# Kernel tuning notes

Hardware: AMD Instinct MI355X
Metric: run time of the kernel (lower is better)

The kernel has to match this reference:

```python
import jax, jax.numpy as jnp
import numpy as np

B, C, RED, H, RANK = 32768, 1024, 4, 4, 16
CH = C // RED          # 256 hidden width after gated down-projection
DH = CH // H           # 64 head dim
RATIO = 0.5            # residual_ratio
LN_EPS = 1e-5


def setup_inputs() -> dict:
    key = jax.random.key(0)
    ks = iter(jax.random.split(key, 32))
    n = lambda shape, s=0.02: jax.random.normal(next(ks), shape, jnp.float32) * s
    return {
        "x": jax.random.normal(next(ks), (B, C), jnp.float32),
        # LayerNorm(c_in)
        "ln_g": jnp.ones((C,), jnp.float32),
        "ln_b": jnp.zeros((C,), jnp.float32),
        # gated linear: down_proj / gate_proj  (stored [in, out])
        "Wd": n((C, CH)), "bd": jnp.zeros((CH,), jnp.float32),
        "Wg": n((C, CH)), "bg": jnp.zeros((CH,), jnp.float32),
        # depthwise Conv1d(CH, CH, k=1, groups=CH) on length-1 seq -> per-channel affine
        "dw_w": n((CH,), 1.0), "dw_b": jnp.zeros((CH,), jnp.float32),
        # LightFNN: Linear-GELU-Linear
        "W1": n((CH, CH)), "b1": jnp.zeros((CH,), jnp.float32),
        "W2": n((CH, CH)), "b2": jnp.zeros((CH,), jnp.float32),
        # MHSA (seq_len = 1)
        "Wq": n((CH, CH)), "bq": jnp.zeros((CH,), jnp.float32),
        "Wk": n((CH, CH)), "bk": jnp.zeros((CH,), jnp.float32),
        "Wv": n((CH, CH)), "bv": jnp.zeros((CH,), jnp.float32),
        "Wo": n((CH, CH)), "bo": jnp.zeros((CH,), jnp.float32),
        # up_proj
        "Wu": n((CH, C)), "bu": jnp.zeros((C,), jnp.float32),
        # LoRA (bias-free)
        "Wld": n((C, RANK)), "Wlu": n((RANK, C)),
    }


def reference(x, ln_g, ln_b, Wd, bd, Wg, bg, dw_w, dw_b,
              W1, b1, W2, b2, Wq, bq, Wk, bk, Wv, bv, Wo, bo,
              Wu, bu, Wld, Wlu):
    residual = x
    # LayerNorm
    mu = jnp.mean(x, axis=-1, keepdims=True)
    var = jnp.mean(jnp.square(x - mu), axis=-1, keepdims=True)
    h = (x - mu) * jax.lax.rsqrt(var + LN_EPS) * ln_g + ln_b
    # gated linear unit
    h = (h @ Wd + bd) * jax.nn.sigmoid(h @ Wg + bg)          # [B, CH]
    # depthwise conv over length-1 sequence == per-channel affine
    h = h * dw_w + dw_b
    # light FFN
    h = jax.nn.gelu(h @ W1 + b1) @ W2 + b2
    # seq_len-1 self-attention: softmax over a single key is 1 => out = Wo(v)
    q = (h @ Wq + bq).reshape(B, H, DH)
    k = (h @ Wk + bk).reshape(B, H, DH)
    v = (h @ Wv + bv).reshape(B, H, DH)
    scores = jnp.sum(q * k, axis=-1, keepdims=True) / jnp.sqrt(jnp.float32(DH))  # [B,H,1]
    attn = jax.nn.softmax(scores, axis=-1)                   # == ones
    h = (attn * v).reshape(B, CH) @ Wo + bo
    # up projection + LoRA
    h = h @ Wu + bu                                          # [B, C]
    h = h + (h @ Wld) @ Wlu
    # dropout is identity at inference; weighted residual mix
    return RATIO * h + (1.0 - RATIO) * residual
```

## Files before the change

kernel.cpp:

```cpp
#include <hip/hip_runtime.h>
#include <hip/hip_bf16.h>
#include <stdint.h>


typedef float f32x4 __attribute__((ext_vector_type(4)));
typedef __bf16 bf16x8 __attribute__((ext_vector_type(8)));
typedef unsigned short u16x8 __attribute__((ext_vector_type(8)));
typedef unsigned short u16x4 __attribute__((ext_vector_type(4)));

#define LN_EPS 1e-5f

__device__ __forceinline__ unsigned short f2bf(float f) {
  unsigned int u = __float_as_uint(f);
  u += 0x7fffu + ((u >> 16) & 1u);
  return (unsigned short)(u >> 16);
}

__device__ __forceinline__ void bar_lds() {
  asm volatile("s_waitcnt lgkmcnt(0)\n\ts_barrier" ::: "memory");
}

__global__ __launch_bounds__(256) void k_prep1(
    const float* __restrict__ ln_g, const float* __restrict__ ln_b,
    const float* __restrict__ Wd, const float* __restrict__ Wg,
    const float* __restrict__ dw_w, const float* __restrict__ dw_b,
    const float* __restrict__ W1, const float* __restrict__ b1,
    const float* __restrict__ W2, const float* __restrict__ b2,
    const float* __restrict__ Wv, const float* __restrict__ Wo,
    const float* __restrict__ Wu,
    unsigned short* __restrict__ PGd, unsigned short* __restrict__ PGg,
    unsigned short* __restrict__ PW1, unsigned short* __restrict__ PWv,
    unsigned short* __restrict__ PWo, unsigned short* __restrict__ PWu,
    float* __restrict__ gdvA, float* __restrict__ ggvA,
    float* __restrict__ bdA, float* __restrict__ bgA,
    float* __restrict__ b1p, float* __restrict__ A0) {
  __shared__ float S[32][257];
  const int b = blockIdx.x, tid = threadIdx.x;

  if (b < 120) {
    const float* src; const float* scale = nullptr; unsigned short* dst;
    int N = 256, kc, NT = 16, nt0 = 0;
    bool csum = false; float* accg_ = nullptr; float* accb_ = nullptr;
    if (b < 32)      { src = Wd; scale = ln_g; dst = PGd; kc = b;      csum = true; accg_ = gdvA; accb_ = bdA; }
    else if (b < 64) { src = Wg; scale = ln_g; dst = PGg; kc = b - 32; csum = true; accg_ = ggvA; accb_ = bgA; }
    else if (b < 72) { src = W1; scale = dw_w; dst = PW1; kc = b - 64; }
    else if (b < 80) { src = Wv; dst = PWv; kc = b - 72; }
    else if (b < 88) { src = Wo; dst = PWo; kc = b - 80; }
    else { int idx = b - 88; kc = idx >> 2; nt0 = (idx & 3) * 16; src = Wu; dst = PWu; N = 1024; NT = 64; }
    const int n0 = nt0 * 16;
    float csg = 0.f, csb = 0.f;
    for (int r = 0; r < 32; ++r) {
      int k = kc * 32 + r;
      float raw = src[(size_t)k * N + n0 + tid];
      float v = scale ? scale[k] * raw : raw;
      S[r][tid] = v;
      if (csum) { csg += v; csb += ln_b[k] * raw; }
    }
    if (csum) { atomicAdd(&accg_[tid], csg); atomicAdd(&accb_[tid], csb); }
    __syncthreads();
    const int ntL = tid >> 4;
    #pragma unroll
    for (int c = 0; c < 4; ++c) {
      int lane = (tid * 4 + c) & 63;
      int kb = (lane >> 4) * 8, nl = ntL * 16 + (lane & 15);
      u16x8 o;
      #pragma unroll
      for (int j = 0; j < 8; ++j) o[j] = f2bf(S[kb + j][nl]);
      *(u16x8*)(dst + ((size_t)(kc * NT + nt0 + ntL) * 64 + lane) * 8) = o;
    }
  } else if (b == 120) {
    float s = 0.f;
    for (int k = 0; k < 256; ++k) s += dw_b[k] * W1[k * 256 + tid];
    b1p[tid] = b1[tid] + s;
  } else {
    int rb = b - 121;
    for (int it = 0; it < 16; ++it) {
      int el = rb * 4096 + it * 256 + tid;
      int row = el >> 8, col = el & 255;
      float v = (row < 256) ? W2[el] : ((row == 256) ? b2[col] : 0.f);
      A0[el] = v;
    }
  }
}

__global__ __launch_bounds__(256) void k_gemm272(
    const float* __restrict__ A, const unsigned short* __restrict__ PB,
    float* __restrict__ C, const float* __restrict__ bias, int NT) {
  __shared__ unsigned short XA[512];
  const int tid = threadIdx.x;
  const int w = tid >> 6, l = tid & 63, q = l >> 4, m15 = l & 15;
  const int r0 = blockIdx.x * 16, ncg = blockIdx.y, N = NT * 16;

  const int srow = tid >> 4, kk = (tid & 15) * 2;
  const int xaidx = ((kk >> 3) * 16 + srow) * 8 + (kk & 7);
  const float* arow = A + (size_t)(r0 + srow) * 256 + kk;

  f32x4 acc[4];
  const f32x4 zero4 = {0.f, 0.f, 0.f, 0.f};
  #pragma unroll
  for (int i = 0; i < 4; ++i) acc[i] = zero4;

  for (int kc = 0; kc < 8; ++kc) {
    float2 v = *(const float2*)(arow + kc * 32);
    u16x4 hv; hv[0] = f2bf(v.x); hv[1] = f2bf(v.y); hv[2] = 0; hv[3] = 0;
    XA[xaidx] = hv[0]; XA[xaidx + 1] = hv[1];
    __syncthreads();
    bf16x8 af = *(const bf16x8*)&XA[l * 8];
    #pragma unroll
    for (int i = 0; i < 4; ++i) {
      bf16x8 bf = *(const bf16x8*)(PB + ((size_t)(kc * NT + ncg * 16 + w * 4 + i) * 64 + l) * 8);
      acc[i] = __builtin_amdgcn_mfma_f32_16x16x32_bf16(af, bf, acc[i], 0, 0, 0);
    }
    __syncthreads();
  }
  #pragma unroll
  for (int i = 0; i < 4; ++i) {
    int col = ncg * 256 + (w * 4 + i) * 16 + m15;
    #pragma unroll
    for (int r = 0; r < 4; ++r) {
      int grow = r0 + q * 4 + r;
      float v = acc[i][r];
      if (grow == 256) v += bias[col];
      C[(size_t)grow * N + col] = v;
    }
  }
}

__global__ __launch_bounds__(256) void k_lora_m4(
    const float* __restrict__ M3, const float* __restrict__ Wld,
    float* __restrict__ M4) {
  __shared__ float RED[256 * 16];
  __shared__ float RED2[16 * 16];
  const int r = blockIdx.x, tid = threadIdx.x;
  const float* mrow = M3 + (size_t)r * 1024;
  float p[16];
  #pragma unroll
  for (int c = 0; c < 16; ++c) p[c] = 0.f;
  #pragma unroll
  for (int k = 0; k < 4; ++k) {
    int n = tid + k * 256;
    float m = mrow[n];
    const float* wl = Wld + n * 16;
    #pragma unroll
    for (int c = 0; c < 16; ++c) p[c] += m * wl[c];
  }
  #pragma unroll
  for (int c = 0; c < 16; ++c) RED[tid * 16 + c] = p[c];
  __syncthreads();
  {
    const int c = tid & 15, g = tid >> 4;
    float s = 0.f;
    #pragma unroll
    for (int i = 0; i < 16; ++i) s += RED[(g * 16 + i) * 16 + c];
    RED2[g * 16 + c] = s;
  }
  __syncthreads();
  if (tid < 16) {
    float s = 0.f;
    #pragma unroll
    for (int g = 0; g < 16; ++g) s += RED2[g * 16 + tid];
    M4[r * 16 + tid] = s;
  }
}

__global__ __launch_bounds__(256) void k_packwc2(
    const float* __restrict__ M3, const float* __restrict__ M4,
    const float* __restrict__ Wlu, unsigned short* __restrict__ PWc,
    float* __restrict__ bcomb) {
  const int b = blockIdx.x, tid = threadIdx.x;
  if (b < 64) {
    __shared__ float M4L[32 * 16];
    __shared__ float WL[16 * 128];
    __shared__ unsigned short TL[32 * 132];
    const int kc = b >> 3, ccol = (b & 7) * 128;
    M4L[tid] = M4[(size_t)kc * 512 + tid];
    M4L[tid + 256] = M4[(size_t)kc * 512 + 256 + tid];
    #pragma unroll
    for (int i = 0; i < 8; ++i) {
      int el = tid + i * 256;
      int s = el >> 7, n = el & 127;
      WL[el] = Wlu[(size_t)s * 1024 + ccol + n];
    }
    __syncthreads();
    const int r = tid >> 3, c0 = (tid & 7) * 16;
    const float* mrow = M3 + (size_t)(kc * 32 + r) * 1024 + ccol + c0;
    float acc[16];
    #pragma unroll
    for (int c = 0; c < 16; ++c) acc[c] = mrow[c];
    #pragma unroll
    for (int s = 0; s < 16; ++s) {
      float m = M4L[r * 16 + s];
      #pragma unroll
      for (int c = 0; c < 16; ++c) acc[c] += m * WL[s * 128 + c0 + c];
    }
    #pragma unroll
    for (int c = 0; c < 16; ++c) TL[r * 132 + c0 + c] = f2bf(acc[c]);
    __syncthreads();
    const int ntL = tid >> 5;
    #pragma unroll
    for (int hlf = 0; hlf < 2; ++hlf) {
      int lane = (tid & 31) + hlf * 32;
      int kb = (lane >> 4) * 8, nl = ntL * 16 + (lane & 15);
      u16x8 o;
      #pragma unroll
      for (int j = 0; j < 8; ++j) o[j] = TL[(kb + j) * 132 + nl];
      *(u16x8*)(PWc + ((size_t)(kc * 64 + (b & 7) * 8 + ntL) * 64 + lane) * 8) = o;
    }
  } else {
    __shared__ float s16[16];
    if (tid < 16) s16[tid] = M4[256 * 16 + tid];
    __syncthreads();
    const float* bc3 = M3 + (size_t)256 * 1024;
    #pragma unroll
    for (int c = 0; c < 4; ++c) {
      int n = tid + c * 256;
      float v = bc3[n];
      #pragma unroll
      for (int s = 0; s < 16; ++s) v += s16[s] * Wlu[s * 1024 + n];
      bcomb[n] = v;
    }
  }
}

__global__ __launch_bounds__(512, 4) void k_main(
    const float* __restrict__ x,
    const unsigned short* __restrict__ PGd, const unsigned short* __restrict__ PGg,
    const unsigned short* __restrict__ PW1, const unsigned short* __restrict__ PWc,
    const float* __restrict__ gdvA, const float* __restrict__ ggvA,
    const float* __restrict__ bdA, const float* __restrict__ bgA,
    const float* __restrict__ bd, const float* __restrict__ bg,
    const float* __restrict__ b1p, const float* __restrict__ bcomb,
    float* __restrict__ out) {
  __shared__ unsigned short XA[2][2048];
  __shared__ unsigned short HBUF[16384];
  __shared__ float SMS[1024];
  __shared__ float MURS[128];
  __shared__ float OBUF[16 * 260];

  const int tid = threadIdx.x;
  const int w = tid >> 6, l = tid & 63, q = l >> 4, m15 = l & 15;
  const int row0 = blockIdx.x * 64;

  float gdc[2], ggc[2], bdc[2], bgc[2], b1c[2];
  #pragma unroll
  for (int i = 0; i < 2; ++i) {
    int col = w * 32 + i * 16 + m15;
    gdc[i] = gdvA[col]; ggc[i] = ggvA[col];
    bdc[i] = bdA[col] + bd[col];
    bgc[i] = bgA[col] + bg[col];
    b1c[i] = b1p[col];
  }

  f32x4 accd[4][2], accg[4][2];
  const f32x4 zero4 = {0.f, 0.f, 0.f, 0.f};
  #pragma unroll
  for (int mt = 0; mt < 4; ++mt)
    #pragma unroll
    for (int i = 0; i < 2; ++i) { accd[mt][i] = zero4; accg[mt][i] = zero4; }

  const int srow = tid >> 3, sseg = tid & 7;
  const float* xrow = x + (size_t)(row0 + srow) * 1024 + sseg * 4;
  const int xaidx = (((srow >> 4) * 64 + (sseg >> 1) * 16 + (srow & 15)) << 3) + (sseg & 1) * 4;
  float ssum = 0.f, ssq = 0.f;

  float4 v = *(const float4*)xrow;
  for (int kc = 0; kc < 32; ++kc) {
    const int p = kc & 1;
    u16x4 hv; hv[0] = f2bf(v.x); hv[1] = f2bf(v.y); hv[2] = f2bf(v.z); hv[3] = f2bf(v.w);
    *(u16x4*)&XA[p][xaidx] = hv;
    ssum += v.x + v.y + v.z + v.w;
    ssq += v.x * v.x + v.y * v.y + v.z * v.z + v.w * v.w;
    if (kc < 31) v = *(const float4*)(xrow + (kc + 1) * 32);
    bar_lds();
    bf16x8 fd[2], fg[2];
    #pragma unroll
    for (int i = 0; i < 2; ++i) {
      size_t off = ((size_t)(kc * 16 + w * 2 + i) * 64 + l) * 8;
      fd[i] = *(const bf16x8*)(PGd + off);
      fg[i] = *(const bf16x8*)(PGg + off);
    }
    #pragma unroll
    for (int mt = 0; mt < 4; ++mt) {
      bf16x8 af = *(const bf16x8*)&XA[p][(mt * 64 + l) * 8];
      #pragma unroll
      for (int i = 0; i < 2; ++i) {
        accd[mt][i] = __builtin_amdgcn_mfma_f32_16x16x32_bf16(af, fd[i], accd[mt][i], 0, 0, 0);
        accg[mt][i] = __builtin_amdgcn_mfma_f32_16x16x32_bf16(af, fg[i], accg[mt][i], 0, 0, 0);
      }
    }
  }

  SMS[tid] = ssum;
  SMS[512 + tid] = ssq;
  bar_lds();
  if (tid < 64) {
    float s = 0.f, sq = 0.f;
    #pragma unroll
    for (int p2 = 0; p2 < 8; ++p2) { s += SMS[tid * 8 + p2]; sq += SMS[512 + tid * 8 + p2]; }
    float mu = s * (1.f / 1024.f);
    float var = sq * (1.f / 1024.f) - mu * mu;
    MURS[tid * 2] = mu;
    MURS[tid * 2 + 1] = rsqrtf(var + LN_EPS);
  }
  bar_lds();

  #pragma unroll
  for (int i = 0; i < 2; ++i) {
    int cloc = i * 16 + m15;
    int q2 = i * 2 + (m15 >> 3), j2 = m15 & 7;
    #pragma unroll
    for (int mt = 0; mt < 4; ++mt) {
      #pragma unroll
      for (int r = 0; r < 4; ++r) {
        int row = mt * 16 + q * 4 + r;
        float mu = MURS[row * 2], rs = MURS[row * 2 + 1];
        float pd = rs * (accd[mt][i][r] - mu * gdc[i]) + bdc[i];
        float pg = rs * (accg[mt][i][r] - mu * ggc[i]) + bgc[i];
        float hv = pd / (1.f + __expf(-pg));
        HBUF[((mt * 8 + w) * 64 + q2 * 16 + q * 4 + r) * 8 + j2] = f2bf(hv);
      }
    }
  }
  bar_lds();

  f32x4 acc2[4][2];
  #pragma unroll
  for (int mt = 0; mt < 4; ++mt)
    #pragma unroll
    for (int i = 0; i < 2; ++i) acc2[mt][i] = zero4;
  for (int kc = 0; kc < 8; ++kc) {
    bf16x8 bf[2];
    #pragma unroll
    for (int i = 0; i < 2; ++i)
      bf[i] = *(const bf16x8*)(PW1 + ((size_t)(kc * 16 + w * 2 + i) * 64 + l) * 8);
    #pragma unroll
    for (int mt = 0; mt < 4; ++mt) {
      bf16x8 af = *(const bf16x8*)&HBUF[((mt * 8 + kc) * 64 + l) * 8];
      #pragma unroll
      for (int i = 0; i < 2; ++i)
        acc2[mt][i] = __builtin_amdgcn_mfma_f32_16x16x32_bf16(af, bf[i], acc2[mt][i], 0, 0, 0);
    }
  }
  bar_lds();
  #pragma unroll
  for (int i = 0; i < 2; ++i) {
    int q2 = i * 2 + (m15 >> 3), j2 = m15 & 7;
    #pragma unroll
    for (int mt = 0; mt < 4; ++mt) {
      #pragma unroll
      for (int r = 0; r < 4; ++r) {
        float vv = acc2[mt][i][r] + b1c[i];
        float u = 0.7978845608f * (vv + 0.044715f * vv * vv * vv);
        float th = 1.f - 2.f / (1.f + __expf(2.f * u));
        HBUF[((mt * 8 + w) * 64 + q2 * 16 + q * 4 + r) * 8 + j2] = f2bf(0.5f * vv * (1.f + th));
      }
    }
  }
  bar_lds();

  for (int nc = 0; nc < 4; ++nc) {
    f32x4 acc3[4][2];
    #pragma unroll
    for (int mt = 0; mt < 4; ++mt)
      #pragma unroll
      for (int i = 0; i < 2; ++i) acc3[mt][i] = zero4;
    for (int kc = 0; kc < 8; ++kc) {
      bf16x8 bf[2];
      #pragma unroll
      for (int i = 0; i < 2; ++i)
        bf[i] = *(const bf16x8*)(PWc + ((size_t)(kc * 64 + nc * 16 + w * 2 + i) * 64 + l) * 8);
      #pragma unroll
      for (int mt = 0; mt < 4; ++mt) {
        bf16x8 af = *(const bf16x8*)&HBUF[((mt * 8 + kc) * 64 + l) * 8];
        #pragma unroll
        for (int i = 0; i < 2; ++i)
          acc3[mt][i] = __builtin_amdgcn_mfma_f32_16x16x32_bf16(af, bf[i], acc3[mt][i], 0, 0, 0);
      }
    }
    float bc[2];
    #pragma unroll
    for (int i = 0; i < 2; ++i) bc[i] = bcomb[nc * 256 + w * 32 + i * 16 + m15];
    const int rowL = tid >> 5, c0 = (tid & 31) * 4;
    #pragma unroll
    for (int mt = 0; mt < 4; ++mt) {
      #pragma unroll
      for (int r = 0; r < 4; ++r)
        #pragma unroll
        for (int i = 0; i < 2; ++i)
          OBUF[(q * 4 + r) * 260 + w * 32 + i * 16 + m15] = acc3[mt][i][r] + bc[i];
      bar_lds();
      const size_t gbase = (size_t)(row0 + mt * 16 + rowL) * 1024 + nc * 256;
      #pragma unroll
      for (int h = 0; h < 2; ++h) {
        int cc = c0 + h * 128;
        f32x4 yv = *(const f32x4*)&OBUF[rowL * 260 + cc];
        float4 xr = *(const float4*)(x + gbase + cc);
        float4 o;
        o.x = 0.5f * yv[0] + 0.5f * xr.x;
        o.y = 0.5f * yv[1] + 0.5f * xr.y;
        o.z = 0.5f * yv[2] + 0.5f * xr.z;
        o.w = 0.5f * yv[3] + 0.5f * xr.w;
        *(float4*)(out + gbase + cc) = o;
      }
      bar_lds();
    }
  }
}

extern "C" void kernel_launch(void* const* d_in, const int* in_sizes, int n_in,
                              void* d_out, int out_size, void* d_ws, size_t ws_size,
                              hipStream_t stream) {
  (void)in_sizes; (void)n_in; (void)out_size; (void)ws_size;
  const float* x    = (const float*)d_in[0];
  const float* ln_g = (const float*)d_in[1];
  const float* ln_b = (const float*)d_in[2];
  const float* Wd   = (const float*)d_in[3];
  const float* bd   = (const float*)d_in[4];
  const float* Wg   = (const float*)d_in[5];
  const float* bg   = (const float*)d_in[6];
  const float* dw_w = (const float*)d_in[7];
  const float* dw_b = (const float*)d_in[8];
  const float* W1   = (const float*)d_in[9];
  const float* b1   = (const float*)d_in[10];
  const float* W2   = (const float*)d_in[11];
  const float* b2   = (const float*)d_in[12];
  const float* Wv   = (const float*)d_in[17];
  const float* bv   = (const float*)d_in[18];
  const float* Wo   = (const float*)d_in[19];
  const float* bo   = (const float*)d_in[20];
  const float* Wu   = (const float*)d_in[21];
  const float* bu   = (const float*)d_in[22];
  const float* Wld  = (const float*)d_in[23];
  const float* Wlu  = (const float*)d_in[24];
  float* out = (float*)d_out;

  char* ws = (char*)d_ws;
  unsigned short* PGd = (unsigned short*)(ws + 0);
  unsigned short* PGg = (unsigned short*)(ws + 524288);
  unsigned short* PW1 = (unsigned short*)(ws + 1048576);
  unsigned short* PWv = (unsigned short*)(ws + 1179648);
  unsigned short* PWo = (unsigned short*)(ws + 1310720);
  unsigned short* PWu = (unsigned short*)(ws + 1441792);
  unsigned short* PWc = (unsigned short*)(ws + 1966080);
  float* gdvA  = (float*)(ws + 2490368);
  float* ggvA  = (float*)(ws + 2491392);
  float* bdA   = (float*)(ws + 2492416);
  float* bgA   = (float*)(ws + 2493440);
  float* b1p   = (float*)(ws + 2494464);
  float* bcomb = (float*)(ws + 2495488);
  float* A0    = (float*)(ws + 2499584);
  float* T1    = (float*)(ws + 2778112);
  float* T2    = A0;
  float* M3    = T1;
  float* M4    = (float*)(ws + 1179648);

  hipMemsetAsync(ws + 2490368, 0, 4096, stream);
  hipLaunchKernelGGL(k_prep1, dim3(138), dim3(256), 0, stream,
                     ln_g, ln_b, Wd, Wg, dw_w, dw_b, W1, b1, W2, b2, Wv, Wo, Wu,
                     PGd, PGg, PW1, PWv, PWo, PWu, gdvA, ggvA, bdA, bgA, b1p, A0);
  hipLaunchKernelGGL(k_gemm272, dim3(17, 1), dim3(256), 0, stream, A0, PWv, T1, bv, 16);
  hipLaunchKernelGGL(k_gemm272, dim3(17, 1), dim3(256), 0, stream, T1, PWo, T2, bo, 16);
  hipLaunchKernelGGL(k_gemm272, dim3(17, 4), dim3(256), 0, stream, T2, PWu, M3, bu, 64);
  hipLaunchKernelGGL(k_lora_m4, dim3(257), dim3(256), 0, stream, M3, Wld, M4);
  hipLaunchKernelGGL(k_packwc2, dim3(65), dim3(256), 0, stream, M3, M4, Wlu, PWc, bcomb);
  hipLaunchKernelGGL(k_main, dim3(512), dim3(512), 0, stream,
                     x, PGd, PGg, PW1, PWc, gdvA, ggvA, bdA, bgA, bd, bg, b1p, bcomb, out);
}
```

Measured before the change: 403.7 us.

## Fuse weight-prep chain into one cooperative kernel with grid syncs

Replaces the memset plus six small prep launches with a single cooperative kernel that uses grid.sync between phases. It reorders the LoRA folding so Wu is combined with Wld/Wlu first, turning the 1024-wide up-projection GEMM into a fold of Wu into WUF. The gate column sums are now written as per-chunk partials and reduced later, replacing atomics and the memset. This cuts launch overhead and serialization in the small weight-preprocessing phase, at the cost of cooperative-launch constraints and some idle blocks across phases.

Measured after the change: 516.9 us. 28.1% more time.

```diff
diff --git a/kernel.cpp b/kernel.cpp
--- a/kernel.cpp
+++ b/kernel.cpp
@@ -1,6 +1,9 @@
 #include <hip/hip_runtime.h>
 #include <hip/hip_bf16.h>
+#include <hip/hip_cooperative_groups.h>
 #include <stdint.h>
+
+namespace cg = cooperative_groups;
 
 
 typedef float f32x4 __attribute__((ext_vector_type(4)));
@@ -20,43 +23,81 @@
   asm volatile("s_waitcnt lgkmcnt(0)\n\ts_barrier" ::: "memory");
 }
 
-__global__ __launch_bounds__(256) void k_prep1(
+__device__ __forceinline__ void gemm16x64(
+    const float* __restrict__ A, const unsigned short* __restrict__ PB,
+    float* __restrict__ C, const float* __restrict__ bias, int b, char* SMEM) {
+  unsigned short* XA = (unsigned short*)SMEM;
+  const int tid = threadIdx.x;
+  const int w = tid >> 6, l = tid & 63, q = l >> 4, m15 = l & 15;
+  const int r0 = (b >> 2) * 16, nt = (b & 3) * 4 + w;
+  const int srow = tid >> 4, kk = (tid & 15) * 2;
+  const int xaidx = ((kk >> 3) * 16 + srow) * 8 + (kk & 7);
+  const float* arow = A + (size_t)(r0 + srow) * 256 + kk;
+  f32x4 acc = {0.f, 0.f, 0.f, 0.f};
+  for (int kc = 0; kc < 8; ++kc) {
+    float2 v = *(const float2*)(arow + kc * 32);
+    XA[xaidx] = f2bf(v.x); XA[xaidx + 1] = f2bf(v.y);
+    __syncthreads();
+    bf16x8 af = *(const bf16x8*)&XA[l * 8];
+    bf16x8 bf = *(const bf16x8*)(PB + ((size_t)(kc * 16 + nt) * 64 + l) * 8);
+    acc = __builtin_amdgcn_mfma_f32_16x16x32_bf16(af, bf, acc, 0, 0, 0);
+    __syncthreads();
+  }
+  const int col = nt * 16 + m15;
+  #pragma unroll
+  for (int r = 0; r < 4; ++r) {
+    int grow = r0 + q * 4 + r;
+    float vv = acc[r];
+    if (grow == 256) vv += bias[col];
+    C[(size_t)grow * 256 + col] = vv;
+  }
+}
+
+__global__ __launch_bounds__(256) void k_prep_all(
     const float* __restrict__ ln_g, const float* __restrict__ ln_b,
     const float* __restrict__ Wd, const float* __restrict__ Wg,
     const float* __restrict__ dw_w, const float* __restrict__ dw_b,
     const float* __restrict__ W1, const float* __restrict__ b1,
     const float* __restrict__ W2, const float* __restrict__ b2,
-    const float* __restrict__ Wv, const float* __restrict__ Wo,
-    const float* __restrict__ Wu,
+    const float* __restrict__ Wv, const float* __restrict__ bv,
+    const float* __restrict__ Wo, const float* __restrict__ bo,
+    const float* __restrict__ Wu, const float* __restrict__ bu,
+    const float* __restrict__ Wld, const float* __restrict__ Wlu,
     unsigned short* __restrict__ PGd, unsigned short* __restrict__ PGg,
     unsigned short* __restrict__ PW1, unsigned short* __restrict__ PWv,
     unsigned short* __restrict__ PWo, unsigned short* __restrict__ PWu,
+    unsigned short* __restrict__ PWc,
     float* __restrict__ gdvA, float* __restrict__ ggvA,
     float* __restrict__ bdA, float* __restrict__ bgA,
-    float* __restrict__ b1p, float* __restrict__ A0) {
-  __shared__ float S[32][257];
+    float* __restrict__ b1p, float* __restrict__ bcomb,
+    float* __restrict__ A0, float* __restrict__ T1,
+    float* __restrict__ WUF, float* __restrict__ P1,
+    float* __restrict__ bu2, float* __restrict__ GP) {
+  __shared__ alignas(16) char SMEM[32896];
+  cg::grid_group grid = cg::this_grid();
   const int b = blockIdx.x, tid = threadIdx.x;
 
-  if (b < 120) {
+  if (b < 88) {
+    float (*S)[257] = (float(*)[257])SMEM;
     const float* src; const float* scale = nullptr; unsigned short* dst;
-    int N = 256, kc, NT = 16, nt0 = 0;
-    bool csum = false; float* accg_ = nullptr; float* accb_ = nullptr;
-    if (b < 32)      { src = Wd; scale = ln_g; dst = PGd; kc = b;      csum = true; accg_ = gdvA; accb_ = bdA; }
-    else if (b < 64) { src = Wg; scale = ln_g; dst = PGg; kc = b - 32; csum = true; accg_ = ggvA; accb_ = bgA; }
+    int kc; int gpa = -1;
+    if (b < 32)      { src = Wd; scale = ln_g; dst = PGd; kc = b;      gpa = 0; }
+    else if (b < 64) { src = Wg; scale = ln_g; dst = PGg; kc = b - 32; gpa = 2; }
     else if (b < 72) { src = W1; scale = dw_w; dst = PW1; kc = b - 64; }
     else if (b < 80) { src = Wv; dst = PWv; kc = b - 72; }
-    else if (b < 88) { src = Wo; dst = PWo; kc = b - 80; }
-    else { int idx = b - 88; kc = idx >> 2; nt0 = (idx & 3) * 16; src = Wu; dst = PWu; N = 1024; NT = 64; }
-    const int n0 = nt0 * 16;
+    else             { src = Wo; dst = PWo; kc = b - 80; }
     float csg = 0.f, csb = 0.f;
     for (int r = 0; r < 32; ++r) {
       int k = kc * 32 + r;
-      float raw = src[(size_t)k * N + n0 + tid];
+      float raw = src[(size_t)k * 256 + tid];
       float v = scale ? scale[k] * raw : raw;
       S[r][tid] = v;
-      if (csum) { csg += v; csb += ln_b[k] * raw; }
-    }
-    if (csum) { atomicAdd(&accg_[tid], csg); atomicAdd(&accb_[tid], csb); }
+      if (gpa >= 0) { csg += v; csb += ln_b[k] * raw; }
+    }
+    if (gpa >= 0) {
+      GP[((size_t)gpa * 32 + kc) * 256 + tid] = csg;
+      GP[((size_t)(gpa + 1) * 32 + kc) * 256 + tid] = csb;
+    }
     __syncthreads();
     const int ntL = tid >> 4;
     #pragma unroll
@@ -66,115 +107,65 @@
       u16x8 o;
       #pragma unroll
       for (int j = 0; j < 8; ++j) o[j] = f2bf(S[kb + j][nl]);
-      *(u16x8*)(dst + ((size_t)(kc * NT + nt0 + ntL) * 64 + lane) * 8) = o;
-    }
-  } else if (b == 120) {
+      *(u16x8*)(dst + ((size_t)(kc * 16 + ntL) * 64 + lane) * 8) = o;
+    }
+  } else if (b == 88) {
     float s = 0.f;
     for (int k = 0; k < 256; ++k) s += dw_b[k] * W1[k * 256 + tid];
     b1p[tid] = b1[tid] + s;
-  } else {
-    int rb = b - 121;
+  } else if (b < 106) {
+    int rb = b - 89;
     for (int it = 0; it < 16; ++it) {
       int el = rb * 4096 + it * 256 + tid;
       int row = el >> 8, col = el & 255;
       float v = (row < 256) ? W2[el] : ((row == 256) ? b2[col] : 0.f);
       A0[el] = v;
     }
-  }
-}
-
-__global__ __launch_bounds__(256) void k_gemm272(
-    const float* __restrict__ A, const unsigned short* __restrict__ PB,
-    float* __restrict__ C, const float* __restrict__ bias, int NT) {
-  __shared__ unsigned short XA[512];
-  const int tid = threadIdx.x;
-  const int w = tid >> 6, l = tid & 63, q = l >> 4, m15 = l & 15;
-  const int r0 = blockIdx.x * 16, ncg = blockIdx.y, N = NT * 16;
-
-  const int srow = tid >> 4, kk = (tid & 15) * 2;
-  const int xaidx = ((kk >> 3) * 16 + srow) * 8 + (kk & 7);
-  const float* arow = A + (size_t)(r0 + srow) * 256 + kk;
-
-  f32x4 acc[4];
-  const f32x4 zero4 = {0.f, 0.f, 0.f, 0.f};
-  #pragma unroll
-  for (int i = 0; i < 4; ++i) acc[i] = zero4;
-
-  for (int kc = 0; kc < 8; ++kc) {
-    float2 v = *(const float2*)(arow + kc * 32);
-    u16x4 hv; hv[0] = f2bf(v.x); hv[1] = f2bf(v.y); hv[2] = 0; hv[3] = 0;
-    XA[xaidx] = hv[0]; XA[xaidx + 1] = hv[1];
-    __syncthreads();
-    bf16x8 af = *(const bf16x8*)&XA[l * 8];
-    #pragma unroll
-    for (int i = 0; i < 4; ++i) {
-      bf16x8 bf = *(const bf16x8*)(PB + ((size_t)(kc * NT + ncg * 16 + w * 4 + i) * 64 + l) * 8);
-      acc[i] = __builtin_amdgcn_mfma_f32_16x16x32_bf16(af, bf, acc[i], 0, 0, 0);
-    }
-    __syncthreads();
-  }
-  #pragma unroll
-  for (int i = 0; i < 4; ++i) {
-    int col = ncg * 256 + (w * 4 + i) * 16 + m15;
-    #pragma unroll
-    for (int r = 0; r < 4; ++r) {
-      int grow = r0 + q * 4 + r;
-      float v = acc[i][r];
-      if (grow == 256) v += bias[col];
-      C[(size_t)grow * N + col] = v;
-    }
-  }
-}
-
-__global__ __launch_bounds__(256) void k_lora_m4(
-    const float* __restrict__ M3, const float* __restrict__ Wld,
-    float* __restrict__ M4) {
-  __shared__ float RED[256 * 16];
-  __shared__ float RED2[16 * 16];
-  const int r = blockIdx.x, tid = threadIdx.x;
-  const float* mrow = M3 + (size_t)r * 1024;
-  float p[16];
-  #pragma unroll
-  for (int c = 0; c < 16; ++c) p[c] = 0.f;
-  #pragma unroll
-  for (int k = 0; k < 4; ++k) {
-    int n = tid + k * 256;
-    float m = mrow[n];
-    const float* wl = Wld + n * 16;
-    #pragma unroll
-    for (int c = 0; c < 16; ++c) p[c] += m * wl[c];
-  }
-  #pragma unroll
-  for (int c = 0; c < 16; ++c) RED[tid * 16 + c] = p[c];
-  __syncthreads();
-  {
-    const int c = tid & 15, g = tid >> 4;
-    float s = 0.f;
-    #pragma unroll
-    for (int i = 0; i < 16; ++i) s += RED[(g * 16 + i) * 16 + c];
-    RED2[g * 16 + c] = s;
-  }
-  __syncthreads();
-  if (tid < 16) {
-    float s = 0.f;
-    #pragma unroll
-    for (int g = 0; g < 16; ++g) s += RED2[g * 16 + tid];
-    M4[r * 16 + tid] = s;
-  }
-}
-
-__global__ __launch_bounds__(256) void k_packwc2(
-    const float* __restrict__ M3, const float* __restrict__ M4,
-    const float* __restrict__ Wlu, unsigned short* __restrict__ PWc,
-    float* __restrict__ bcomb) {
-  const int b = blockIdx.x, tid = threadIdx.x;
-  if (b < 64) {
-    __shared__ float M4L[32 * 16];
-    __shared__ float WL[16 * 128];
-    __shared__ unsigned short TL[32 * 132];
-    const int kc = b >> 3, ccol = (b & 7) * 128;
-    M4L[tid] = M4[(size_t)kc * 512 + tid];
-    M4L[tid + 256] = M4[(size_t)kc * 512 + 256 + tid];
+  } else if (b < 363) {
+    float* RED = (float*)SMEM;
+    float* RED2 = RED + 4096;
+    const int r = b - 106;
+    const float* mrow = (r < 256) ? (Wu + (size_t)r * 1024) : bu;
+    float p[16];
+    #pragma unroll
+    for (int c = 0; c < 16; ++c) p[c] = 0.f;
+    #pragma unroll
+    for (int k = 0; k < 4; ++k) {
+      int n = tid + k * 256;
+      float m = mrow[n];
+      const float* wl = Wld + (size_t)n * 16;
+      #pragma unroll
+      for (int c = 0; c < 16; ++c) p[c] += m * wl[c];
+    }
+    #pragma unroll
+    for (int c = 0; c < 16; ++c) RED[tid * 16 + c] = p[c];
+    __syncthreads();
+    {
+      const int c = tid & 15, g2 = tid >> 4;
+      float s = 0.f;
+      #pragma unroll
+      for (int i = 0; i < 16; ++i) s += RED[(g2 * 16 + i) * 16 + c];
+      RED2[g2 * 16 + c] = s;
+    }
+    __syncthreads();
+    if (tid < 16) {
+      float s = 0.f;
+      #pragma unroll
+      for (int g3 = 0; g3 < 16; ++g3) s += RED2[g3 * 16 + tid];
+      P1[r * 16 + tid] = s;
+    }
+  }
+  grid.sync();
+
+  if (b < 68) {
+    gemm16x64(A0, PWv, T1, bv, b, SMEM);
+  } else if (b < 132) {
+    const int fb = b - 68, kcb = fb >> 3, ccol = (fb & 7) * 128;
+    float* P1L = (float*)SMEM;
+    float* WL = P1L + 512;
+    unsigned short* TL = (unsigned short*)(WL + 2048);
+    P1L[tid] = P1[(size_t)kcb * 512 + tid];
+    P1L[tid + 256] = P1[(size_t)kcb * 512 + 256 + tid];
     #pragma unroll
     for (int i = 0; i < 8; ++i) {
       int el = tid + i * 256;
@@ -183,15 +174,25 @@
     }
     __syncthreads();
     const int r = tid >> 3, c0 = (tid & 7) * 16;
-    const float* mrow = M3 + (size_t)(kc * 32 + r) * 1024 + ccol + c0;
+    const float* wrow = Wu + (size_t)(kcb * 32 + r) * 1024 + ccol + c0;
     float acc[16];
     #pragma unroll
-    for (int c = 0; c < 16; ++c) acc[c] = mrow[c];
+    for (int cc = 0; cc < 4; ++cc) {
+      f32x4 wv = *(const f32x4*)(wrow + cc * 4);
+      #pragma unroll
+      for (int j = 0; j < 4; ++j) acc[cc * 4 + j] = wv[j];
+    }
     #pragma unroll
     for (int s = 0; s < 16; ++s) {
-      float m = M4L[r * 16 + s];
+      float m = P1L[r * 16 + s];
       #pragma unroll
       for (int c = 0; c < 16; ++c) acc[c] += m * WL[s * 128 + c0 + c];
+    }
+    float* wout = WUF + (size_t)(kcb * 32 + r) * 1024 + ccol + c0;
+    #pragma unroll
+    for (int cc = 0; cc < 4; ++cc) {
+      f32x4 ov = {acc[cc * 4], acc[cc * 4 + 1], acc[cc * 4 + 2], acc[cc * 4 + 3]};
+      *(f32x4*)(wout + cc * 4) = ov;
     }
     #pragma unroll
     for (int c = 0; c < 16; ++c) TL[r * 132 + c0 + c] = f2bf(acc[c]);
@@ -204,21 +205,88 @@
       u16x8 o;
       #pragma unroll
       for (int j = 0; j < 8; ++j) o[j] = TL[(kb + j) * 132 + nl];
-      *(u16x8*)(PWc + ((size_t)(kc * 64 + (b & 7) * 8 + ntL) * 64 + lane) * 8) = o;
-    }
-  } else {
-    __shared__ float s16[16];
-    if (tid < 16) s16[tid] = M4[256 * 16 + tid];
-    __syncthreads();
-    const float* bc3 = M3 + (size_t)256 * 1024;
+      *(u16x8*)(PWu + ((size_t)(kcb * 64 + (fb & 7) * 8 + ntL) * 64 + lane) * 8) = o;
+    }
+  } else if (b == 132) {
+    float* s16 = (float*)SMEM;
+    if (tid < 16) s16[tid] = P1[256 * 16 + tid];
+    __syncthreads();
     #pragma unroll
     for (int c = 0; c < 4; ++c) {
       int n = tid + c * 256;
-      float v = bc3[n];
+      float v = bu[n];
       #pragma unroll
       for (int s = 0; s < 16; ++s) v += s16[s] * Wlu[s * 1024 + n];
-      bcomb[n] = v;
-    }
+      bu2[n] = v;
+    }
+  } else if (b == 133) {
+    float s0 = 0.f, s1 = 0.f, s2 = 0.f, s3 = 0.f;
+    for (int kc2 = 0; kc2 < 32; ++kc2) {
+      s0 += GP[((size_t)0 * 32 + kc2) * 256 + tid];
+      s1 += GP[((size_t)1 * 32 + kc2) * 256 + tid];
+      s2 += GP[((size_t)2 * 32 + kc2) * 256 + tid];
+      s3 += GP[((size_t)3 * 32 + kc2) * 256 + tid];
+    }
+    gdvA[tid] = s0; bdA[tid] = s1; ggvA[tid] = s2; bgA[tid] = s3;
+  }
+  grid.sync();
+
+  if (b < 68) gemm16x64(T1, PWo, A0, bo, b, SMEM);
+  grid.sync();
+
+  const float* T2 = A0;
+  if (b < 128) {
+    unsigned short* XA2 = (unsigned short*)SMEM;
+    unsigned short* TL = XA2 + 2048;
+    const int rb = b >> 4, cg = b & 15;
+    const int w = tid >> 6, l = tid & 63, q = l >> 4, m15 = l & 15;
+    const int r0 = rb * 32;
+    const int srow = tid >> 3;
+    const int kk = (tid & 7) * 4;
+    const int rt = srow >> 4, m = srow & 15;
+    const int xaidx = rt * 512 + ((kk >> 3) * 16 + m) * 8 + (kk & 7);
+    const float* arow = T2 + (size_t)(r0 + srow) * 256 + kk;
+    f32x4 acc0 = {0.f, 0.f, 0.f, 0.f}, acc1 = {0.f, 0.f, 0.f, 0.f};
+    float4 v = *(const float4*)arow;
+    for (int kc = 0; kc < 8; ++kc) {
+      unsigned short* xp = XA2 + (kc & 1) * 1024;
+      u16x4 hv; hv[0] = f2bf(v.x); hv[1] = f2bf(v.y); hv[2] = f2bf(v.z); hv[3] = f2bf(v.w);
+      *(u16x4*)&xp[xaidx] = hv;
+      if (kc < 7) v = *(const float4*)(arow + (kc + 1) * 32);
+      bar_lds();
+      bf16x8 bf = *(const bf16x8*)(PWu + ((size_t)(kc * 64 + cg * 4 + w) * 64 + l) * 8);
+      bf16x8 af0 = *(const bf16x8*)&xp[l * 8];
+      bf16x8 af1 = *(const bf16x8*)&xp[512 + l * 8];
+      acc0 = __builtin_amdgcn_mfma_f32_16x16x32_bf16(af0, bf, acc0, 0, 0, 0);
+      acc1 = __builtin_amdgcn_mfma_f32_16x16x32_bf16(af1, bf, acc1, 0, 0, 0);
+    }
+    #pragma unroll
+    for (int r = 0; r < 4; ++r) {
+      TL[(q * 4 + r) * 68 + w * 16 + m15] = f2bf(acc0[r]);
+      TL[(16 + q * 4 + r) * 68 + w * 16 + m15] = f2bf(acc1[r]);
+    }
+    bar_lds();
+    const int ntL = tid >> 6, lane = tid & 63;
+    const int kb = (lane >> 4) * 8, nl = ntL * 16 + (lane & 15);
+    u16x8 o;
+    #pragma unroll
+    for (int j = 0; j < 8; ++j) o[j] = TL[(kb + j) * 68 + nl];
+    *(u16x8*)(PWc + ((size_t)(rb * 64 + cg * 4 + ntL) * 64 + lane) * 8) = o;
+  } else if (b < 144) {
+    float* T2row = (float*)SMEM;
+    float* PB4 = T2row + 256;
+    const int c0 = (b - 128) * 64;
+    T2row[tid] = T2[(size_t)256 * 256 + tid];
+    __syncthreads();
+    const int kpart = tid >> 6, cl = tid & 63, c = c0 + cl;
+    float s = 0.f;
+    for (int k = kpart * 64; k < kpart * 64 + 64; ++k)
+      s += T2row[k] * WUF[(size_t)k * 1024 + c];
+    PB4[kpart * 64 + cl] = s;
+    __syncthreads();
+    if (tid < 64)
+      bcomb[c0 + tid] = PB4[tid] + PB4[64 + tid] + PB4[128 + tid] + PB4[192 + tid]
+                        + bu2[c0 + tid];
   }
 }
 
@@ -306,7 +374,6 @@
 
   #pragma unroll
   for (int i = 0; i < 2; ++i) {
-    int cloc = i * 16 + m15;
     int q2 = i * 2 + (m15 >> 3), j2 = m15 & 7;
     #pragma unroll
     for (int mt = 0; mt < 4; ++mt) {
@@ -450,19 +517,25 @@
   float* bcomb = (float*)(ws + 2495488);
   float* A0    = (float*)(ws + 2499584);
   float* T1    = (float*)(ws + 2778112);
-  float* T2    = A0;
-  float* M3    = T1;
-  float* M4    = (float*)(ws + 1179648);
-
-  hipMemsetAsync(ws + 2490368, 0, 4096, stream);
-  hipLaunchKernelGGL(k_prep1, dim3(138), dim3(256), 0, stream,
-                     ln_g, ln_b, Wd, Wg, dw_w, dw_b, W1, b1, W2, b2, Wv, Wo, Wu,
-                     PGd, PGg, PW1, PWv, PWo, PWu, gdvA, ggvA, bdA, bgA, b1p, A0);
-  hipLaunchKernelGGL(k_gemm272, dim3(17, 1), dim3(256), 0, stream, A0, PWv, T1, bv, 16);
-  hipLaunchKernelGGL(k_gemm272, dim3(17, 1), dim3(256), 0, stream, T1, PWo, T2, bo, 16);
-  hipLaunchKernelGGL(k_gemm272, dim3(17, 4), dim3(256), 0, stream, T2, PWu, M3, bu, 64);
-  hipLaunchKernelGGL(k_lora_m4, dim3(257), dim3(256), 0, stream, M3, Wld, M4);
-  hipLaunchKernelGGL(k_packwc2, dim3(65), dim3(256), 0, stream, M3, M4, Wlu, PWc, bcomb);
+  float* WUF   = (float*)(ws + 3056640);
+  float* bu2   = (float*)(ws + 4105216);
+  float* GP    = (float*)(ws + 1966080);
+  float* P1    = (float*)(ws + 1966080 + 131072);
+
+  void* args[] = {
+      (void*)&ln_g, (void*)&ln_b, (void*)&Wd, (void*)&Wg,
+      (void*)&dw_w, (void*)&dw_b, (void*)&W1, (void*)&b1,
+      (void*)&W2, (void*)&b2, (void*)&Wv, (void*)&bv,
+      (void*)&Wo, (void*)&bo, (void*)&Wu, (void*)&bu,
+      (void*)&Wld, (void*)&Wlu,
+      (void*)&PGd, (void*)&PGg, (void*)&PW1, (void*)&PWv,
+      (void*)&PWo, (void*)&PWu, (void*)&PWc,
+      (void*)&gdvA, (void*)&ggvA, (void*)&bdA, (void*)&bgA,
+      (void*)&b1p, (void*)&bcomb,
+      (void*)&A0, (void*)&T1, (void*)&WUF, (void*)&P1,
+      (void*)&bu2, (void*)&GP};
+  hipLaunchCooperativeKernel((const void*)k_prep_all, dim3(363), dim3(256),
+                             args, 0, stream);
   hipLaunchKernelGGL(k_main, dim3(512), dim3(512), 0, stream,
                      x, PGd, PGg, PW1, PWc, gdvA, ggvA, bdA, bgA, bd, bg, b1p, bcomb, out);
 }
```
